# Kernel optimization log

Hardware: AMD Instinct MI355X
Metric: run time of the kernel (lower is better)

The kernel has to match this reference:

```python
import jax, jax.numpy as jnp
import numpy as np

B = 2_097_152  # batch of (ttm, logm) option quotes
J = 5          # hidden width from hidden_sizes=[5,5,5]


def setup_inputs() -> dict:
    key = jax.random.key(0)
    ks = jax.random.split(key, 14)
    d = jnp.float32
    s = 0.01  # torch init: normal(mean=0, std=0.01)
    inp = {
        "ttm": jax.random.uniform(ks[0], (B, 1), d),
        "logm": jax.random.normal(ks[1], (B, 1), d),
        "weights_logm": jax.random.normal(ks[2], (1, J), d) * s,
        "bias_logm": jax.random.normal(ks[3], (1, J), d) * s,
        "weights_ttm": jax.random.normal(ks[4], (1, J), d) * s,
        "bias_ttm": jax.random.normal(ks[5], (1, J), d) * s,
        "weights_exp": jax.random.normal(ks[6], (J, 1), d) * s,
        "bias_exp": jax.random.normal(ks[7], (1, J), d) * s,
        # nn.Linear default init ~ U(-1/sqrt(J), 1/sqrt(J))
        "W1": jax.random.uniform(ks[8], (J, J), d, -1.0, 1.0) / np.sqrt(J),
        "b1": jax.random.uniform(ks[9], (J,), d, -1.0, 1.0) / np.sqrt(J),
        "W2": jax.random.uniform(ks[10], (J, J), d, -1.0, 1.0) / np.sqrt(J),
        "b2": jax.random.uniform(ks[11], (J,), d, -1.0, 1.0) / np.sqrt(J),
        "Wo": jax.random.uniform(ks[12], (1, J), d, -1.0, 1.0) / np.sqrt(J),
        "bo": jax.random.uniform(ks[13], (1,), d, -1.0, 1.0) / np.sqrt(J),
    }
    return inp


def _forward(ttm, logm, weights_logm, bias_logm, weights_ttm, bias_ttm,
             weights_exp, bias_exp, W1, b1, W2, b2, Wo, bo):
    # smile transform of log-moneyness: sqrt(x*tanh(x+0.5) + tanh(-x/2) + 5e-4)
    x = bias_logm + logm @ jnp.exp(weights_logm)                     # [B, J]
    term_logm = jnp.sqrt(x * jnp.tanh(x + 0.5) + jnp.tanh(-x / 2) + 0.0005)
    term_ttm = jax.nn.sigmoid(bias_ttm + ttm @ jnp.exp(weights_ttm))  # [B, J]
    h = (term_logm * term_ttm) @ jnp.exp(weights_exp) + bias_exp      # [B,1]+[1,J] -> [B, J]
    h = jax.nn.softplus(h @ W1.T + b1)
    h = jax.nn.softplus(h @ W2.T + b2)
    return h @ Wo.T + bo                                              # [B, 1]


def reference(ttm, logm, weights_logm, bias_logm, weights_ttm, bias_ttm,
              weights_exp, bias_exp, W1, b1, W2, b2, Wo, bo):
    params = (weights_logm, bias_logm, weights_ttm, bias_ttm,
              weights_exp, bias_exp, W1, b1, W2, b2, Wo, bo)

    def out_sum(t, l):
        return jnp.sum(_forward(t, l, *params))

    output = _forward(ttm, logm, *params)                 # [B, 1]
    # grad of sum(output) wrt ttm and logm (rows independent -> per-sample grads)
    grad_ttm1, grad_logm1 = jax.grad(out_sum, argnums=(0, 1))(ttm, logm)
    # second derivative wrt logm: grad of sum(grad_logm1)
    grad_logm2 = jax.grad(
        lambda l: jnp.sum(jax.grad(out_sum, argnums=1)(ttm, l))
    )(logm)
    return (output, grad_ttm1, grad_logm1, grad_logm2)
```

## Files before the change

kernel.cpp:

```cpp
#include <hip/hip_runtime.h>
#include <math.h>

#define J 5
#define LOG2E 1.4426950408889634f
#define LN2   0.6931471805599453f

#if defined(__HIP_DEVICE_COMPILE__) && __has_builtin(__builtin_amdgcn_rcpf)
__device__ __forceinline__ float fastrcp(float x) { return __builtin_amdgcn_rcpf(x); }
#else
__device__ __forceinline__ float fastrcp(float x) { return 1.0f / x; }
#endif

#if defined(__HIP_DEVICE_COMPILE__) && __has_builtin(__builtin_amdgcn_rsqf)
__device__ __forceinline__ float fastrsq(float x) { return __builtin_amdgcn_rsqf(x); }
#else
__device__ __forceinline__ float fastrsq(float x) { return 1.0f / sqrtf(x); }
#endif

#if defined(__HIP_DEVICE_COMPILE__) && __has_builtin(__builtin_amdgcn_exp2f)
__device__ __forceinline__ float fexp2(float x) { return __builtin_amdgcn_exp2f(x); }
#else
__device__ __forceinline__ float fexp2(float x) { return exp2f(x); }
#endif

#if defined(__HIP_DEVICE_COMPILE__) && __has_builtin(__builtin_amdgcn_logf)
__device__ __forceinline__ float flog2(float x) { return __builtin_amdgcn_logf(x); }
#else
__device__ __forceinline__ float flog2(float x) { return log2f(x); }
#endif

__global__ void setup_kernel(const float* __restrict__ w_logm, const float* __restrict__ b_logm,
                             const float* __restrict__ w_ttm,  const float* __restrict__ b_ttm,
                             const float* __restrict__ w_exp,  const float* __restrict__ b_exp,
                             const float* __restrict__ W1,     const float* __restrict__ b1,
                             const float* __restrict__ W2,     const float* __restrict__ b2,
                             const float* __restrict__ Wo,     const float* __restrict__ bo,
                             float* __restrict__ c)
{
    const int j = threadIdx.x;
    if (j >= J) return;
    const float ewl = __expf(w_logm[j]);
    const float ewt = __expf(w_ttm[j]);
    const float ewe = __expf(w_exp[j]);
    c[0  + j] = ewl * LOG2E;
    c[5  + j] = b_logm[j] * LOG2E;
    c[10 + j] = ewl;
    c[15 + j] = -ewt * LOG2E;
    c[20 + j] = -b_ttm[j] * LOG2E;
    c[25 + j] = ewe;
    c[30 + j] = ewt * ewe;
    float r = 0.0f, cc = b1[j];
#pragma unroll
    for (int t = 0; t < J; ++t) {
        const float w = W1[j * J + t];
        r += w;
        cc = fmaf(w, b_exp[t], cc);
    }
    c[35 + j] = r;
    c[40 + j] = r * LOG2E;
    c[45 + j] = cc * LOG2E;
    c[50 + j] = r * r;
#pragma unroll
    for (int t = 0; t < J; ++t) c[55 + j * J + t] = W2[j * J + t];
    c[80 + j] = b2[j] * LOG2E;
    c[85 + j] = Wo[j];
    c[90 + j] = Wo[j] * LN2;
    if (j == 0) c[95] = bo[0];
}

__global__ __launch_bounds__(256, 6) void smile_main(
    const float* __restrict__ ttm, const float* __restrict__ logm,
    const float* __restrict__ c, float* __restrict__ out, int n)
{
    const int tid = blockIdx.x * blockDim.x + threadIdx.x;
    if (tid >= n) return;

    const float T = ttm[tid];
    const float L = logm[tid];

    float ewlb[J], blb[J], ewl[J], newtb[J], nbtb[J], ewe[J], wte[J];
#pragma unroll
    for (int j = 0; j < J; ++j) {
        ewlb[j]  = c[0  + j];
        blb[j]   = c[5  + j];
        ewl[j]   = c[10 + j];
        newtb[j] = c[15 + j];
        nbtb[j]  = c[20 + j];
        ewe[j]   = c[25 + j];
        wte[j]   = c[30 + j];
    }

    float s = 0.0f, sL = 0.0f, sLL = 0.0f, sT = 0.0f;
#pragma unroll
    for (int j = 0; j < J; ++j) {
        const float x2 = fmaf(L, ewlb[j], blb[j]);
        const float ex = fexp2(x2);
        const float x  = x2 * LN2;
        const float e2 = ex * ex;
        const float w1 = fastrcp(fmaf(2.7182818284590452f, e2, 1.0f));
        const float t1 = fmaf(-2.0f, w1, 1.0f);
        const float w2 = fastrcp(1.0f + ex);
        const float t2 = fmaf(2.0f, w2, -1.0f);
        const float m1 = fmaf(-t1, t1, 1.0f);
        const float m2 = fmaf(-t2, t2, 1.0f);
        const float u  = fmaf(x, t1, t2 + 5.0e-4f);
        const float xm1 = x * m1;
        const float ux  = fmaf(-0.5f, m2, t1 + xm1);
        const float f1  = fmaf(-t1, xm1, m1);
        const float uxx = fmaf(-0.5f * t2, m2, f1 + f1);
        const float r   = fastrsq(u);
        const float tl  = u * r;
        const float i2  = 0.5f * r;
        const float h   = ux * (r * r);
        const float tt  = fastrcp(1.0f + fexp2(fmaf(T, newtb[j], nbtb[j])));
        const float dtt = fmaf(-tt, tt, tt);
        const float AA   = tt * ewe[j];
        const float ewlA = ewl[j] * AA;
        s  = fmaf(tl, AA, s);
        const float G = ux * i2;
        sL = fmaf(G, ewlA, sL);
        const float inner = fmaf(-0.5f * ux, h, uxx);
        sLL = fmaf(inner * i2, ewl[j] * ewlA, sLL);
        sT  = fmaf(tl * dtt, wte[j], sT);
    }

    float r1[J], r1b[J], c1b[J], r1sq[J], W2r[J * J], b2b[J], wo[J], wob[J];
#pragma unroll
    for (int j = 0; j < J; ++j) {
        r1[j]   = c[35 + j];
        r1b[j]  = c[40 + j];
        c1b[j]  = c[45 + j];
        r1sq[j] = c[50 + j];
        b2b[j]  = c[80 + j];
        wo[j]   = c[85 + j];
        wob[j]  = c[90 + j];
    }
#pragma unroll
    for (int t = 0; t < J * J; ++t) W2r[t] = c[55 + t];
    const float bo0 = c[95];

    float sp2[J], q[J], p[J];
#pragma unroll
    for (int i = 0; i < J; ++i) {
        const float a2 = fmaf(s, r1b[i], c1b[i]);
        const float ex = fexp2(a2);
        const float d  = 1.0f + ex;
        const float w  = fastrcp(d);
        const float sg = 1.0f - w;
        sp2[i] = flog2(d);
        q[i]   = sg * r1[i];
        p[i]   = (w * sg) * r1sq[i];
    }

    float o = bo0, u1 = 0.0f, u2 = 0.0f, u3 = 0.0f;
#pragma unroll
    for (int i = 0; i < J; ++i) {
        float g2 = b2b[i], Bq = 0.0f, Bp = 0.0f;
#pragma unroll
        for (int j = 0; j < J; ++j) {
            const float w = W2r[i * J + j];
            g2 = fmaf(w, sp2[j], g2);
            Bq = fmaf(w, q[j],   Bq);
            Bp = fmaf(w, p[j],   Bp);
        }
        const float ex = fexp2(g2);
        const float d  = 1.0f + ex;
        const float w  = fastrcp(d);
        const float sg = 1.0f - w;
        const float dsg = w * sg;
        o  = fmaf(wob[i], flog2(d), o);
        const float t = wo[i] * sg;
        u1 = fmaf(t, Bq, u1);
        u2 = fmaf(t, Bp, u2);
        u3 = fmaf(wo[i] * dsg, Bq * Bq, u3);
    }

    const size_t nn = (size_t)n;
    out[tid]          = o;
    out[nn + tid]     = sT * u1;
    out[2 * nn + tid] = sL * u1;
    out[3 * nn + tid] = fmaf(sL * sL, u3 + u2, sLL * u1);
}

extern "C" void kernel_launch(void* const* d_in, const int* in_sizes, int n_in,
                              void* d_out, int out_size, void* d_ws, size_t ws_size,
                              hipStream_t stream) {
    const float* ttm    = (const float*)d_in[0];
    const float* logm   = (const float*)d_in[1];
    const float* w_logm = (const float*)d_in[2];
    const float* b_logm = (const float*)d_in[3];
    const float* w_ttm  = (const float*)d_in[4];
    const float* b_ttm  = (const float*)d_in[5];
    const float* w_exp  = (const float*)d_in[6];
    const float* b_exp  = (const float*)d_in[7];
    const float* W1     = (const float*)d_in[8];
    const float* b1     = (const float*)d_in[9];
    const float* W2     = (const float*)d_in[10];
    const float* b2     = (const float*)d_in[11];
    const float* Wo     = (const float*)d_in[12];
    const float* bo     = (const float*)d_in[13];
    float* out = (float*)d_out;
    float* cns = (float*)d_ws;

    const int n = in_sizes[0];
    setup_kernel<<<1, 64, 0, stream>>>(w_logm, b_logm, w_ttm, b_ttm, w_exp, b_exp,
                                       W1, b1, W2, b2, Wo, bo, cns);
    const int blocks = (n + 255) / 256;
    smile_main<<<blocks, 256, 0, stream>>>(ttm, logm, cns, out, n);
}
```

Baseline: 121.7 us.

## Process two samples per thread with packed float2 math and vector loads

Each thread now handles two consecutive samples as float2 vectors, so elementwise FMAs and multiplies can map to packed FP32 instructions on CDNA. Loads and stores become 64-bit. The two tanh reciprocals are merged into one reciprocal of their product. Transcendentals stay scalar. Risks are higher register pressure under the existing launch bounds, and odd n is mishandled because the tail check and vector access assume n is even.

```diff
diff --git a/kernel.cpp b/kernel.cpp
--- a/kernel.cpp
+++ b/kernel.cpp
@@ -5,6 +5,8 @@
 #define LOG2E 1.4426950408889634f
 #define LN2   0.6931471805599453f
 
+typedef float v2f __attribute__((ext_vector_type(2)));
+
 #if defined(__HIP_DEVICE_COMPILE__) && __has_builtin(__builtin_amdgcn_rcpf)
 __device__ __forceinline__ float fastrcp(float x) { return __builtin_amdgcn_rcpf(x); }
 #else
@@ -28,6 +30,15 @@
 #else
 __device__ __forceinline__ float flog2(float x) { return log2f(x); }
 #endif
+
+__device__ __forceinline__ v2f v2s(float a) { return (v2f){a, a}; }
+__device__ __forceinline__ v2f vfma(v2f a, v2f b, v2f c) { return __builtin_elementwise_fma(a, b, c); }
+__device__ __forceinline__ v2f vfma(v2f a, float b, v2f c) { return __builtin_elementwise_fma(a, v2s(b), c); }
+__device__ __forceinline__ v2f vfma(v2f a, float b, float c) { return __builtin_elementwise_fma(a, v2s(b), v2s(c)); }
+__device__ __forceinline__ v2f v2exp2(v2f x) { return (v2f){fexp2(x.x), fexp2(x.y)}; }
+__device__ __forceinline__ v2f v2rcp (v2f x) { return (v2f){fastrcp(x.x), fastrcp(x.y)}; }
+__device__ __forceinline__ v2f v2rsq (v2f x) { return (v2f){fastrsq(x.x), fastrsq(x.y)}; }
+__device__ __forceinline__ v2f v2log2(v2f x) { return (v2f){flog2(x.x), flog2(x.y)}; }
 
 __global__ void setup_kernel(const float* __restrict__ w_logm, const float* __restrict__ b_logm,
                              const float* __restrict__ w_ttm,  const float* __restrict__ b_ttm,
@@ -73,10 +84,10 @@
     const float* __restrict__ c, float* __restrict__ out, int n)
 {
     const int tid = blockIdx.x * blockDim.x + threadIdx.x;
-    if (tid >= n) return;
-
-    const float T = ttm[tid];
-    const float L = logm[tid];
+    if (tid * 2 >= n) return;
+
+    const v2f T = ((const v2f*)ttm)[tid];
+    const v2f L = ((const v2f*)logm)[tid];
 
     float ewlb[J], blb[J], ewl[J], newtb[J], nbtb[J], ewe[J], wte[J];
 #pragma unroll
@@ -90,38 +101,40 @@
         wte[j]   = c[30 + j];
     }
 
-    float s = 0.0f, sL = 0.0f, sLL = 0.0f, sT = 0.0f;
+    v2f s = v2s(0.0f), sL = v2s(0.0f), sLL = v2s(0.0f), sT = v2s(0.0f);
 #pragma unroll
     for (int j = 0; j < J; ++j) {
-        const float x2 = fmaf(L, ewlb[j], blb[j]);
-        const float ex = fexp2(x2);
-        const float x  = x2 * LN2;
-        const float e2 = ex * ex;
-        const float w1 = fastrcp(fmaf(2.7182818284590452f, e2, 1.0f));
-        const float t1 = fmaf(-2.0f, w1, 1.0f);
-        const float w2 = fastrcp(1.0f + ex);
-        const float t2 = fmaf(2.0f, w2, -1.0f);
-        const float m1 = fmaf(-t1, t1, 1.0f);
-        const float m2 = fmaf(-t2, t2, 1.0f);
-        const float u  = fmaf(x, t1, t2 + 5.0e-4f);
-        const float xm1 = x * m1;
-        const float ux  = fmaf(-0.5f, m2, t1 + xm1);
-        const float f1  = fmaf(-t1, xm1, m1);
-        const float uxx = fmaf(-0.5f * t2, m2, f1 + f1);
-        const float r   = fastrsq(u);
-        const float tl  = u * r;
-        const float i2  = 0.5f * r;
-        const float h   = ux * (r * r);
-        const float tt  = fastrcp(1.0f + fexp2(fmaf(T, newtb[j], nbtb[j])));
-        const float dtt = fmaf(-tt, tt, tt);
-        const float AA   = tt * ewe[j];
-        const float ewlA = ewl[j] * AA;
-        s  = fmaf(tl, AA, s);
-        const float G = ux * i2;
-        sL = fmaf(G, ewlA, sL);
-        const float inner = fmaf(-0.5f * ux, h, uxx);
-        sLL = fmaf(inner * i2, ewl[j] * ewlA, sLL);
-        sT  = fmaf(tl * dtt, wte[j], sT);
+        const v2f x2 = vfma(L, ewlb[j], v2s(blb[j]));
+        const v2f ex = v2exp2(x2);
+        const v2f x  = x2 * LN2;
+        const v2f e2 = ex * ex;
+        const v2f a   = vfma(e2, 2.7182818284590452f, 1.0f);
+        const v2f b   = ex + 1.0f;
+        const v2f rab = v2rcp(a * b);
+        const v2f w1  = b * rab;
+        const v2f w2  = a * rab;
+        const v2f t1  = vfma(w1, -2.0f, 1.0f);
+        const v2f t2  = vfma(w2,  2.0f, -1.0f);
+        const v2f m1  = vfma(-t1, t1, v2s(1.0f));
+        const v2f m2  = vfma(-t2, t2, v2s(1.0f));
+        const v2f u   = vfma(x, t1, t2 + 5.0e-4f);
+        const v2f xm1 = x * m1;
+        const v2f ux  = vfma(m2, -0.5f, t1 + xm1);
+        const v2f f1  = vfma(-t1, xm1, m1);
+        const v2f uxx = vfma(t2 * (-0.5f), m2, f1 + f1);
+        const v2f r   = v2rsq(u);
+        const v2f tl  = u * r;
+        const v2f i2  = r * 0.5f;
+        const v2f h   = ux * (r * r);
+        const v2f tt  = v2rcp(v2exp2(vfma(T, newtb[j], v2s(nbtb[j]))) + 1.0f);
+        const v2f dtt = vfma(-tt, tt, tt);
+        const v2f AA   = tt * ewe[j];
+        const v2f ewlA = AA * ewl[j];
+        s  = vfma(tl, AA, s);
+        sL = vfma(ux * i2, ewlA, sL);
+        const v2f inner = vfma(ux * (-0.5f), h, uxx);
+        sLL = vfma(inner * i2, ewlA * ewl[j], sLL);
+        sT  = vfma(tl * dtt, wte[j], sT);
     }
 
     float r1[J], r1b[J], c1b[J], r1sq[J], W2r[J * J], b2b[J], wo[J], wob[J];
@@ -139,47 +152,47 @@
     for (int t = 0; t < J * J; ++t) W2r[t] = c[55 + t];
     const float bo0 = c[95];
 
-    float sp2[J], q[J], p[J];
+    v2f sp2[J], q[J], p[J];
 #pragma unroll
     for (int i = 0; i < J; ++i) {
-        const float a2 = fmaf(s, r1b[i], c1b[i]);
-        const float ex = fexp2(a2);
-        const float d  = 1.0f + ex;
-        const float w  = fastrcp(d);
-        const float sg = 1.0f - w;
-        sp2[i] = flog2(d);
+        const v2f a2 = vfma(s, r1b[i], v2s(c1b[i]));
+        const v2f ex = v2exp2(a2);
+        const v2f d  = ex + 1.0f;
+        const v2f w  = v2rcp(d);
+        const v2f sg = v2s(1.0f) - w;
+        sp2[i] = v2log2(d);
         q[i]   = sg * r1[i];
         p[i]   = (w * sg) * r1sq[i];
     }
 
-    float o = bo0, u1 = 0.0f, u2 = 0.0f, u3 = 0.0f;
+    v2f o = v2s(bo0), u1 = v2s(0.0f), u2 = v2s(0.0f), u3 = v2s(0.0f);
 #pragma unroll
     for (int i = 0; i < J; ++i) {
-        float g2 = b2b[i], Bq = 0.0f, Bp = 0.0f;
+        v2f g2 = v2s(b2b[i]), Bq = v2s(0.0f), Bp = v2s(0.0f);
 #pragma unroll
         for (int j = 0; j < J; ++j) {
             const float w = W2r[i * J + j];
-            g2 = fmaf(w, sp2[j], g2);
-            Bq = fmaf(w, q[j],   Bq);
-            Bp = fmaf(w, p[j],   Bp);
+            g2 = vfma(sp2[j], w, g2);
+            Bq = vfma(q[j],   w, Bq);
+            Bp = vfma(p[j],   w, Bp);
         }
-        const float ex = fexp2(g2);
-        const float d  = 1.0f + ex;
-        const float w  = fastrcp(d);
-        const float sg = 1.0f - w;
-        const float dsg = w * sg;
-        o  = fmaf(wob[i], flog2(d), o);
-        const float t = wo[i] * sg;
-        u1 = fmaf(t, Bq, u1);
-        u2 = fmaf(t, Bp, u2);
-        u3 = fmaf(wo[i] * dsg, Bq * Bq, u3);
+        const v2f ex  = v2exp2(g2);
+        const v2f d   = ex + 1.0f;
+        const v2f w   = v2rcp(d);
+        const v2f sg  = v2s(1.0f) - w;
+        const v2f dsg = w * sg;
+        o  = vfma(v2log2(d), wob[i], o);
+        const v2f t = sg * wo[i];
+        u1 = vfma(t, Bq, u1);
+        u2 = vfma(t, Bp, u2);
+        u3 = vfma(dsg * wo[i], Bq * Bq, u3);
     }
 
     const size_t nn = (size_t)n;
-    out[tid]          = o;
-    out[nn + tid]     = sT * u1;
-    out[2 * nn + tid] = sL * u1;
-    out[3 * nn + tid] = fmaf(sL * sL, u3 + u2, sLL * u1);
+    ((v2f*)(out))[tid]          = o;
+    ((v2f*)(out + nn))[tid]     = sT * u1;
+    ((v2f*)(out + 2 * nn))[tid] = sL * u1;
+    ((v2f*)(out + 3 * nn))[tid] = vfma(sL * sL, u3 + u2, sLL * u1);
 }
 
 extern "C" void kernel_launch(void* const* d_in, const int* in_sizes, int n_in,
@@ -205,6 +218,7 @@
     const int n = in_sizes[0];
     setup_kernel<<<1, 64, 0, stream>>>(w_logm, b_logm, w_ttm, b_ttm, w_exp, b_exp,
                                        W1, b1, W2, b2, Wo, bo, cns);
-    const int blocks = (n + 255) / 256;
+    const int threads = (n + 1) / 2;
+    const int blocks  = (threads + 255) / 256;
     smile_main<<<blocks, 256, 0, stream>>>(ttm, logm, cns, out, n);
 }
```

New measurement: 112.3 us. -7.7%, faster.
